# Optimization experiments

Measured on AMD Instinct MI355X. Metric: run time of the kernel, lower is better.

Reference implementation:

```python
import jax, jax.numpy as jnp
import numpy as np

B, N, D, YD = 256, 1024, 64, 2
EPS = 1e-7  # keras SCC epsilon clip


def interleave(x):
    # (B, L, ...): out[:,0::2]=first half, out[:,1::2]=second half
    b, L = x.shape[0], x.shape[1]
    a, c = x[:, : L // 2], x[:, L // 2:]
    return jnp.stack([a, c], axis=2).reshape((b, L) + x.shape[2:])


def block_interleave(x, scope):
    # tf.split into N//scope chunks of size `scope`, Interleave each, concat
    b, L = x.shape[0], x.shape[1]
    rest = x.shape[2:]
    xr = x.reshape((b, L // scope, 2, scope // 2) + rest)
    xr = jnp.swapaxes(xr, 2, 3)
    return xr.reshape((b, L) + rest)


def split_even_odd(x):
    # returns (odd, even) = (x[:,0::2], x[:,1::2])
    return x[:, 0::2], x[:, 1::2]


def mlp2(x, W1, b1, W2, b2):
    return jnp.dot(jax.nn.relu(jnp.dot(x, W1) + b1), W2) + b2


def emb2llr(e, W, b):
    return jax.nn.softmax(jnp.dot(e, W) + b, axis=-1)


def scce(v, p):
    # v: (B,L,1) int labels, p: (B,L,2) probs -> (B,L) per-element NLL
    pt = jnp.take_along_axis(p, v, axis=-1)[..., 0]
    return -jnp.log(jnp.clip(pt, EPS, 1.0))


def setup_inputs() -> dict:
    key = jax.random.key(0)
    ks = jax.random.split(key, 16)
    s = lambda fan: 1.0 / np.sqrt(fan)
    return {
        "x": jax.random.randint(ks[0], (B, N, 1), 0, 2, dtype=jnp.int32),
        "y": jax.random.normal(ks[1], (B, N, YD), dtype=jnp.float32),
        "emb_W": jax.random.normal(ks[2], (YD, D), dtype=jnp.float32) * s(YD),
        "emb_b": jnp.zeros((D,), jnp.float32),
        "lab_emb": jax.random.normal(ks[3], (2, D), dtype=jnp.float32) * s(D),
        "cn_W1": jax.random.normal(ks[4], (2 * D, D), dtype=jnp.float32) * s(2 * D),
        "cn_b1": jnp.zeros((D,), jnp.float32),
        "cn_W2": jax.random.normal(ks[5], (D, D), dtype=jnp.float32) * s(D),
        "cn_b2": jnp.zeros((D,), jnp.float32),
        "bn_W1": jax.random.normal(ks[6], (3 * D, D), dtype=jnp.float32) * s(3 * D),
        "bn_b1": jnp.zeros((D,), jnp.float32),
        "bn_W2": jax.random.normal(ks[7], (D, D), dtype=jnp.float32) * s(D),
        "bn_b2": jnp.zeros((D,), jnp.float32),
        "llr_W": jax.random.normal(ks[8], (D, 2), dtype=jnp.float32) * s(D),
        "llr_b": jnp.zeros((2,), jnp.float32),
    }


def reference(x, y, emb_W, emb_b, lab_emb, cn_W1, cn_b1, cn_W2, cn_b2,
              bn_W1, bn_b1, bn_W2, bn_b2, llr_W, llr_b):
    v = x.astype(jnp.int32)  # (B,N,1)
    e = jnp.dot(y, emb_W) + emb_b  # (B,N,D) observation embedding

    losses, preds, norms = [], [], []
    pred = emb2llr(e, llr_W, llr_b)
    losses.append(scce(v, pred))
    preds.append(pred)
    norms.append(jnp.linalg.norm(e, axis=-1))

    scope = 2
    while scope <= N:
        v_il = block_interleave(v, scope)
        v_odd, v_even = split_even_odd(v_il)
        v_xor = jnp.mod(v_odd + v_even, 2)  # (B,N/2,1)
        v_prime = interleave(jnp.concatenate((v_xor, v_even), axis=1))

        e_il = block_interleave(e, scope)
        e_odd, e_even = split_even_odd(e_il)  # (B,N/2,D) each
        v_xor_emb = lab_emb[v_xor[..., 0]]  # (B,N/2,D)

        e1_left = mlp2(jnp.concatenate((e_odd, e_even), axis=-1),
                       cn_W1, cn_b1, cn_W2, cn_b2)
        e1_right = mlp2(jnp.concatenate((e_odd, e_even, v_xor_emb), axis=-1),
                        bn_W1, bn_b1, bn_W2, bn_b2)
        e_prime = interleave(jnp.concatenate((e1_left, e1_right), axis=1))

        pred = emb2llr(e_prime, llr_W, llr_b)
        losses.append(scce(v_prime, pred))
        preds.append(pred)
        norms.append(jnp.linalg.norm(e_prime, axis=-1))

        v, e = v_prime, e_prime
        scope *= 2

    return (jnp.stack(losses, axis=-2),   # (B, S, N)
            jnp.stack(preds, axis=-2),    # (B, N, S, 2)
            jnp.stack(norms, axis=-2))    # (B, S, N)
```

## Files before the change

kernel.cpp:

```cpp
#include <hip/hip_runtime.h>
#include <hip/hip_bf16.h>

#define NB 256
#define NN 1024
#define NSTAGES 11
#define EPSF 1e-7f

typedef unsigned short u16;
typedef unsigned int u32;
typedef unsigned long long u64;
typedef __attribute__((ext_vector_type(8))) short short8;
typedef __attribute__((ext_vector_type(16))) float f32x16;

static constexpr size_t PRED_BASE = (size_t)NB * NSTAGES * NN;
static constexpr size_t NORM_BASE = PRED_BASE + (size_t)NB * NN * NSTAGES * 2;

static constexpr int LW_OFF = 24576;

#define WLDS_FR 30

static constexpr size_t STAGE_OFF = 131072;
static constexpr size_t PRED_F2_PER_B = (size_t)NSTAGES * NN;
static constexpr size_t PRED_BYTES = (size_t)NB * NSTAGES * NN * 2 * sizeof(float);
static constexpr size_t E9_OFF = STAGE_OFF + PRED_BYTES;
static constexpr size_t E9_BYTES = (size_t)512 * 65536;
static constexpr size_t VM_OFF = E9_OFF + E9_BYTES;
static constexpr size_t NEED_SPLIT = VM_OFF + (size_t)512 * 16 * sizeof(u32);
static constexpr size_t NEED_STAGED = STAGE_OFF + PRED_BYTES;

__device__ __forceinline__ u16 f2bf(float f) {
  unsigned u = __float_as_uint(f);
  unsigned r = (u + 0x7fffu + ((u >> 16) & 1u)) >> 16;
  return (u16)r;
}
__device__ __forceinline__ unsigned pack_bf2(float a, float b) {
  __hip_bfloat162 h = __float22bfloat162_rn(make_float2(a, b));
  return *(unsigned*)&h;
}
__device__ __forceinline__ u32 spread16(u32 v) {
  v = (v | (v << 8)) & 0x00FF00FFu;
  v = (v | (v << 4)) & 0x0F0F0F0Fu;
  v = (v | (v << 2)) & 0x33333333u;
  v = (v | (v << 1)) & 0x55555555u;
  return v;
}
template <bool STAGED>
__device__ __forceinline__ void emit_out(float* __restrict__ out, float* __restrict__ pred_ws,
                                         int b, int n, int s,
                                         float z0, float z1, float nrm2, int label) {
  float m  = fmaxf(z0, z1);
  float p0 = expf(z0 - m), p1 = expf(z1 - m);
  float inv = 1.0f / (p0 + p1);
  p0 *= inv; p1 *= inv;
  float pt = label ? p1 : p0;
  pt = fminf(fmaxf(pt, EPSF), 1.0f);
  out[((size_t)b * NSTAGES + s) * NN + n] = -logf(pt);
  if (STAGED) {
    ((float2*)pred_ws)[((size_t)b * NSTAGES + s) * NN + n] = make_float2(p0, p1);
  } else {
    size_t pb = PRED_BASE + (((size_t)b * NN + n) * NSTAGES + s) * 2;
    out[pb + 0] = p0;
    out[pb + 1] = p1;
  }
  out[NORM_BASE + ((size_t)b * NSTAGES + s) * NN + n] = sqrtf(nrm2);
}

__device__ __forceinline__ int eaddr(int row, int c16) {
  return row * 64 + (((c16) ^ (row & 7)) << 3);
}
__device__ __forceinline__ int eaddr32(int row, int m31) {
  return row * 64 + (((((m31) >> 2) ^ (row & 7)) << 3) | (((m31) & 3) << 1));
}

__global__ __launch_bounds__(256) void prep_kernel(
    const float* __restrict__ cn_W1, const float* __restrict__ bn_W1,
    const float* __restrict__ cn_W2, const float* __restrict__ bn_W2,
    const float* __restrict__ lab_emb, const float* __restrict__ llr_W,
    const float* __restrict__ bn_b1,
    u16* __restrict__ wfrag, float* __restrict__ labW_g) {
  int t = blockIdx.x * 256 + threadIdx.x;
  if (t < 3072) {
    int f = t >> 6, l = t & 63, h = l >> 5, c = l & 31;
    const float* src; int ks, nt;
    if (f < 16)      { src = cn_W1; ks = f >> 1; nt = f & 1; }
    else if (f < 32) { int g = f - 16; src = bn_W1; ks = g >> 1; nt = g & 1; }
    else if (f < 40) { int g = f - 32; src = cn_W2; ks = g >> 1; nt = g & 1; }
    else             { int g = f - 40; src = bn_W2; ks = g >> 1; nt = g & 1; }
    int col = 2 * c + nt;
    u16 vals[8];
    #pragma unroll
    for (int j = 0; j < 8; ++j) {
      int k = ks * 16 + h * 8 + j;
      vals[j] = f2bf(src[k * 64 + col]);
    }
    uint4 u;
    u.x = (unsigned)vals[0] | ((unsigned)vals[1] << 16);
    u.y = (unsigned)vals[2] | ((unsigned)vals[3] << 16);
    u.z = (unsigned)vals[4] | ((unsigned)vals[5] << 16);
    u.w = (unsigned)vals[6] | ((unsigned)vals[7] << 16);
    *(uint4*)(wfrag + (size_t)t * 8) = u;
  } else if (t < 3136) {
    int k = t - 3072;
    unsigned wv = (unsigned)f2bf(llr_W[k * 2]) | ((unsigned)f2bf(llr_W[k * 2 + 1]) << 16);
    ((unsigned*)(wfrag + LW_OFF))[k] = wv;
  } else if (t < 3264) {
    int idx = t - 3136;
    int v = idx >> 6, c = idx & 63;
    float acc = bn_b1[c];
    for (int d = 0; d < 64; ++d)
      acc = fmaf(lab_emb[v * 64 + d], bn_W1[(128 + d) * 64 + c], acc);
    labW_g[idx] = acc;
  }
}

__global__ __launch_bounds__(512) void pred_transpose_kernel(
    const float* __restrict__ pred_ws, float* __restrict__ out) {
  __shared__ float2 tb[NSTAGES * 1026];
  const int tid = threadIdx.x;
  const int b = blockIdx.x;
  const float2* src = (const float2*)pred_ws + (size_t)b * PRED_F2_PER_B;
  for (int i = tid; i < NSTAGES * NN; i += 512) {
    int s = i >> 10, n = i & (NN - 1);
    tb[s * 1026 + n] = src[i];
  }
  __syncthreads();
  float2* dst = (float2*)(out + PRED_BASE) + (size_t)b * PRED_F2_PER_B;
  for (int j = tid; j < NSTAGES * NN; j += 512) {
    int n = j / NSTAGES, s = j - n * NSTAGES;
    dst[j] = tb[s * 1026 + n];
  }
}

#define AFR(FI) (*(const short8*)(wlds + (FI) * 512 + ln * 8))
#define BFR(FI) (((FI) < WLDS_FR) ? *(const short8*)(wlds + (FI) * 512 + ln * 8) \
                                  : *(const short8*)(wfrag + (size_t)(FI) * 512 + ln * 8))

__global__ __launch_bounds__(512, 2) void polar_a_kernel(
    const int* __restrict__ x, const float* __restrict__ y,
    const float* __restrict__ emb_W, const float* __restrict__ emb_b,
    const u16* __restrict__ wfrag, const float* __restrict__ labW_g,
    const float* __restrict__ cn_b1, const float* __restrict__ cn_b2,
    const float* __restrict__ bn_b2, const float* __restrict__ llr_W,
    const float* __restrict__ llr_b, float* __restrict__ pred_ws,
    u16* __restrict__ e9_ws, u32* __restrict__ vm_ws,
    float* __restrict__ out) {
  __shared__ __align__(16) u16 eLh[512 * 64];
  __shared__ __align__(16) u16 wlds[48 * 512];
  __shared__ u32 lwL[64];
  __shared__ u32 vmask[2][16];
  __shared__ float labW[2][64];

  const int tid = threadIdx.x;
  const int w = tid >> 6, ln = tid & 63;
  const int m31 = ln & 31, h8 = ln >> 5;
  const int b = blockIdx.x >> 1, h = blockIdx.x & 1;

  for (int i = tid; i < 48 * 64; i += 512)
    ((uint4*)wlds)[i] = ((const uint4*)wfrag)[i];
  if (tid < 64) lwL[tid] = ((const u32*)(wfrag + LW_OFF))[tid];
  if (tid < 128) ((float*)labW)[tid] = labW_g[tid];

  const float lb0 = llr_b[0], lb1 = llr_b[1];
  const float2 cb1 = *(const float2*)(cn_b1 + 2 * m31);
  const float2 cb2 = *(const float2*)(cn_b2 + 2 * m31);
  const float2 bb2 = *(const float2*)(bn_b2 + 2 * m31);

  {
    int nl = tid;
    int n = 512 * h + nl;
    float2 yv = *(const float2*)(y + ((size_t)b * NN + n) * 2);
    float z0 = lb0, z1 = lb1, nr = 0.f;
    #pragma unroll
    for (int o8 = 0; o8 < 8; ++o8) {
      u32 vals[4];
      #pragma unroll
      for (int jj = 0; jj < 4; ++jj) {
        int o = o8 * 8 + jj * 2;
        float e0 = fmaf(yv.x, emb_W[o],     fmaf(yv.y, emb_W[64 + o],     emb_b[o]));
        float e1 = fmaf(yv.x, emb_W[o + 1], fmaf(yv.y, emb_W[64 + o + 1], emb_b[o + 1]));
        vals[jj] = pack_bf2(e0, e1);
        z0 = fmaf(e0, llr_W[o * 2 + 0], z0); z1 = fmaf(e0, llr_W[o * 2 + 1], z1);
        nr = fmaf(e0, e0, nr);
        z0 = fmaf(e1, llr_W[o * 2 + 2], z0); z1 = fmaf(e1, llr_W[o * 2 + 3], z1);
        nr = fmaf(e1, e1, nr);
      }
      uint4 q; q.x = vals[0]; q.y = vals[1]; q.z = vals[2]; q.w = vals[3];
      *(uint4*)(eLh + eaddr(nl, o8)) = q;
    }
    int v = x[(size_t)b * NN + n] & 1;
    emit_out<true>(out, pred_ws, b, n, 0, z0, z1, nr, v);
    u64 bm = __ballot(v != 0);
    if (ln == 0)  vmask[0][2 * w]     = (u32)bm;
    if (ln == 32) vmask[0][2 * w + 1] = (u32)(bm >> 32);
  }
  __syncthreads();

  const float2 lwv0 = *(const float2*)(&labW[0][2 * m31]);
  const float2 lwv1 = *(const float2*)(&labW[1][2 * m31]);

  #pragma unroll 1
  for (int s = 1; s <= 9; ++s) {
    const int sh = s - 1;
    const int half = 1 << sh;
    const u32* vmR = vmask[(s - 1) & 1];
    u32* vmW = vmask[s & 1];

    short8 Ao[4], Ae[4];
    int iog, ieg, iol, iel, vo, ve, vx;
    u32 bxs;
    {
      int i = 256 * h + 32 * w + m31;
      int g = i >> sh, u = i & (half - 1);
      iog = g * (half << 1) + u;
      ieg = iog + half;
      iol = iog & 511; iel = ieg & 511;
      #pragma unroll
      for (int f = 0; f < 4; ++f) {
        Ao[f] = *(const short8*)(eLh + eaddr(iol, f * 2 + h8));
        Ae[f] = *(const short8*)(eLh + eaddr(iel, f * 2 + h8));
      }
      vo = (vmR[iol >> 5] >> (iol & 31)) & 1;
      ve = (vmR[iel >> 5] >> (iel & 31)) & 1;
      vx = vo ^ ve;
      u32 bx = (u32)__ballot(vx != 0);
      u32 be = (u32)__ballot(ve != 0);
      bxs = bx;
      u32 lo = spread16(bx & 0xffffu) | (spread16(be & 0xffffu) << 1);
      u32 hi = spread16(bx >> 16) | (spread16(be >> 16) << 1);
      if (ln == 0) { vmW[2 * w] = lo; vmW[2 * w + 1] = hi; }
    }
    __syncthreads();

    if (s >= 2) {
      const uint4* lwq = (const uint4*)lwL;
      uint4 lq[4][2];
      #pragma unroll
      for (int f = 0; f < 4; ++f) {
        lq[f][0] = lwq[f * 4 + h8 * 2];
        lq[f][1] = lwq[f * 4 + h8 * 2 + 1];
      }
      #pragma unroll
      for (int side = 0; side < 2; ++side) {
        float z0 = 0.f, z1 = 0.f, nr = 0.f;
        #pragma unroll
        for (int f = 0; f < 4; ++f) {
          short8 av8 = side ? Ae[f] : Ao[f];
          #pragma unroll
          for (int j = 0; j < 8; ++j) {
            u32 pv = ((const u32*)&av8)[j >> 1];
            float val = __uint_as_float((j & 1) ? (pv & 0xffff0000u) : (pv << 16));
            u32 lwp = (j < 4) ? ((const u32*)&lq[f][0])[j] : ((const u32*)&lq[f][1])[j - 4];
            z0 = fmaf(val, __uint_as_float(lwp << 16), z0);
            z1 = fmaf(val, __uint_as_float(lwp & 0xffff0000u), z1);
            nr = fmaf(val, val, nr);
          }
        }
        z0 += __shfl_xor(z0, 32);
        z1 += __shfl_xor(z1, 32);
        nr += __shfl_xor(nr, 32);
        if (h8 == 0)
          emit_out<true>(out, pred_ws, b, side ? ieg : iog, s - 1,
                         z0 + lb0, z1 + lb1, nr, side ? ve : vo);
      }
    }

    f32x16 a0, a1;
    #pragma unroll
    for (int r = 0; r < 16; ++r) { a0[r] = cb1.x; a1[r] = cb1.y; }
    #pragma unroll
    for (int ks = 0; ks < 8; ++ks) {
      short8 B0 = AFR(ks * 2 + 0);
      short8 B1 = AFR(ks * 2 + 1);
      short8 a = (ks < 4) ? Ao[ks] : Ae[ks - 4];
      a0 = __builtin_amdgcn_mfma_f32_32x32x16_bf16(a, B0, a0, 0, 0, 0);
      a1 = __builtin_amdgcn_mfma_f32_32x32x16_bf16(a, B1, a1, 0, 0, 0);
    }
    {
      int obase = 64 * w;
      #pragma unroll
      for (int r = 0; r < 16; ++r) {
        int row = (r & 3) + 8 * (r >> 2) + 4 * h8;
        int R = obase + 2 * row;
        *(u32*)(eLh + eaddr32(R, m31)) =
            pack_bf2(fmaxf(a0[r], 0.f), fmaxf(a1[r], 0.f));
      }
    }

    #pragma unroll
    for (int r = 0; r < 16; ++r) {
      int row = (r & 3) + 8 * (r >> 2) + 4 * h8;
      int bit = (bxs >> row) & 1;
      a0[r] = bit ? lwv1.x : lwv0.x;
      a1[r] = bit ? lwv1.y : lwv0.y;
    }
    #pragma unroll
    for (int ks = 0; ks < 8; ++ks) {
      short8 B0 = AFR(16 + ks * 2 + 0);
      short8 B1 = AFR(16 + ks * 2 + 1);
      short8 a = (ks < 4) ? Ao[ks] : Ae[ks - 4];
      a0 = __builtin_amdgcn_mfma_f32_32x32x16_bf16(a, B0, a0, 0, 0, 0);
      a1 = __builtin_amdgcn_mfma_f32_32x32x16_bf16(a, B1, a1, 0, 0, 0);
    }
    {
      int obase = 64 * w;
      #pragma unroll
      for (int r = 0; r < 16; ++r) {
        int row = (r & 3) + 8 * (r >> 2) + 4 * h8;
        int R = obase + 2 * row + 1;
        *(u32*)(eLh + eaddr32(R, m31)) =
            pack_bf2(fmaxf(a0[r], 0.f), fmaxf(a1[r], 0.f));
      }
    }

    {
      short8 Hc[4];
      {
        int R = 64 * w + 2 * m31;
        #pragma unroll
        for (int f = 0; f < 4; ++f)
          Hc[f] = *(const short8*)(eLh + eaddr(R, f * 2 + h8));
      }
      f32x16 d0, d1;
      #pragma unroll
      for (int r = 0; r < 16; ++r) { d0[r] = cb2.x; d1[r] = cb2.y; }
      #pragma unroll
      for (int ks = 0; ks < 4; ++ks) {
        short8 B0 = AFR(32 + ks * 2 + 0);
        short8 B1 = AFR(32 + ks * 2 + 1);
        d0 = __builtin_amdgcn_mfma_f32_32x32x16_bf16(Hc[ks], B0, d0, 0, 0, 0);
        d1 = __builtin_amdgcn_mfma_f32_32x32x16_bf16(Hc[ks], B1, d1, 0, 0, 0);
      }
      int obase = 64 * w;
      #pragma unroll
      for (int r = 0; r < 16; ++r) {
        int row = (r & 3) + 8 * (r >> 2) + 4 * h8;
        int R = obase + 2 * row;
        *(u32*)(eLh + eaddr32(R, m31)) = pack_bf2(d0[r], d1[r]);
      }
    }

    {
      short8 Hb[4];
      {
        int R = 64 * w + 2 * m31 + 1;
        #pragma unroll
        for (int f = 0; f < 4; ++f)
          Hb[f] = *(const short8*)(eLh + eaddr(R, f * 2 + h8));
      }
      f32x16 d0, d1;
      #pragma unroll
      for (int r = 0; r < 16; ++r) { d0[r] = bb2.x; d1[r] = bb2.y; }
      #pragma unroll
      for (int ks = 0; ks < 4; ++ks) {
        short8 B0 = AFR(40 + ks * 2 + 0);
        short8 B1 = AFR(40 + ks * 2 + 1);
        d0 = __builtin_amdgcn_mfma_f32_32x32x16_bf16(Hb[ks], B0, d0, 0, 0, 0);
        d1 = __builtin_amdgcn_mfma_f32_32x32x16_bf16(Hb[ks], B1, d1, 0, 0, 0);
      }
      int obase = 64 * w;
      #pragma unroll
      for (int r = 0; r < 16; ++r) {
        int row = (r & 3) + 8 * (r >> 2) + 4 * h8;
        int R = obase + 2 * row + 1;
        *(u32*)(eLh + eaddr32(R, m31)) = pack_bf2(d0[r], d1[r]);
      }
    }
    __syncthreads();
  }

  {
    const uint4* src = (const uint4*)eLh;
    uint4* dst = (uint4*)(e9_ws + (size_t)(b * 2 + h) * 32768);
    for (int i = tid; i < 4096; i += 512) dst[i] = src[i];
    if (tid < 16) vm_ws[(b * 2 + h) * 16 + tid] = vmask[1][tid];
  }
}

__global__ __launch_bounds__(512, 2) void polar_b_kernel(
    const u16* __restrict__ wfrag, const float* __restrict__ labW_g,
    const float* __restrict__ cn_b1, const float* __restrict__ cn_b2,
    const float* __restrict__ bn_b2, const float* __restrict__ llr_b,
    float* __restrict__ pred_ws, const u16* __restrict__ e9_ws,
    const u32* __restrict__ vm_ws, float* __restrict__ out) {
  __shared__ __align__(16) u16 eL[NN * 64];
  __shared__ __align__(16) u16 wlds[WLDS_FR * 512];
  __shared__ u32 lwL[64];
  __shared__ u32 vmA[32];
  __shared__ u32 vmB[32];
  __shared__ float labW[2][64];

  const int tid = threadIdx.x;
  const int w = tid >> 6, ln = tid & 63;
  const int m31 = ln & 31, h8 = ln >> 5;
  const int b = blockIdx.x;

  for (int i = tid; i < WLDS_FR * 64; i += 512)
    ((uint4*)wlds)[i] = ((const uint4*)wfrag)[i];
  if (tid < 64) lwL[tid] = ((const u32*)(wfrag + LW_OFF))[tid];
  if (tid < 128) ((float*)labW)[tid] = labW_g[tid];
  if (tid < 32) vmA[tid] = vm_ws[b * 32 + tid];

  const float lb0 = llr_b[0], lb1 = llr_b[1];
  const float2 cb1 = *(const float2*)(cn_b1 + 2 * m31);
  const float2 cb2 = *(const float2*)(cn_b2 + 2 * m31);
  const float2 bb2 = *(const float2*)(bn_b2 + 2 * m31);
  __syncthreads();

  const float2 lwv0 = *(const float2*)(&labW[0][2 * m31]);
  const float2 lwv1 = *(const float2*)(&labW[1][2 * m31]);

  const u16* e9a = e9_ws + (size_t)(b * 2 + 0) * 32768;
  const u16* e9b = e9_ws + (size_t)(b * 2 + 1) * 32768;

  short8 Ao[2][4], Ae[2][4];
  int io[2], ie[2], vo[2], ve[2], vx[2];
  u32 bxs[2];
  #pragma unroll
  for (int t = 0; t < 2; ++t) {
    int i = 64 * w + 32 * t + m31;
    io[t] = i; ie[t] = i + 512;
    #pragma unroll
    for (int f = 0; f < 4; ++f) {
      Ao[t][f] = *(const short8*)(e9a + eaddr(i, f * 2 + h8));
      Ae[t][f] = *(const short8*)(e9b + eaddr(i, f * 2 + h8));
    }
    vo[t] = (vmA[i >> 5] >> (i & 31)) & 1;
    ve[t] = (vmA[(i >> 5) + 16] >> (i & 31)) & 1;
    vx[t] = vo[t] ^ ve[t];
    u32 bx = (u32)__ballot(vx[t] != 0);
    u32 be = (u32)__ballot(ve[t] != 0);
    bxs[t] = bx;
    u32 lo = spread16(bx & 0xffffu) | (spread16(be & 0xffffu) << 1);
    u32 hi = spread16(bx >> 16) | (spread16(be >> 16) << 1);
    if (ln == 0) { vmB[4 * w + 2 * t] = lo; vmB[4 * w + 2 * t + 1] = hi; }
  }
  __syncthreads();

  {
    const uint4* lwq = (const uint4*)lwL;
    uint4 lq[4][2];
    #pragma unroll
    for (int f = 0; f < 4; ++f) {
      lq[f][0] = lwq[f * 4 + h8 * 2];
      lq[f][1] = lwq[f * 4 + h8 * 2 + 1];
    }
    #pragma unroll
    for (int t = 0; t < 2; ++t) {
      #pragma unroll
      for (int side = 0; side < 2; ++side) {
        float z0 = 0.f, z1 = 0.f, nr = 0.f;
        #pragma unroll
        for (int f = 0; f < 4; ++f) {
          short8 av8 = side ? Ae[t][f] : Ao[t][f];
          #pragma unroll
          for (int j = 0; j < 8; ++j) {
            u32 pv = ((const u32*)&av8)[j >> 1];
            float val = __uint_as_float((j & 1) ? (pv & 0xffff0000u) : (pv << 16));
            u32 lwp = (j < 4) ? ((const u32*)&lq[f][0])[j] : ((const u32*)&lq[f][1])[j - 4];
            z0 = fmaf(val, __uint_as_float(lwp << 16), z0);
            z1 = fmaf(val, __uint_as_float(lwp & 0xffff0000u), z1);
            nr = fmaf(val, val, nr);
          }
        }
        z0 += __shfl_xor(z0, 32);
        z1 += __shfl_xor(z1, 32);
        nr += __shfl_xor(nr, 32);
        if (h8 == 0)
          emit_out<true>(out, pred_ws, b, side ? ie[t] : io[t], 9,
                         z0 + lb0, z1 + lb1, nr, side ? ve[t] : vo[t]);
      }
    }
  }

  f32x16 a0[2], a1[2];
  #pragma unroll
  for (int t = 0; t < 2; ++t)
    #pragma unroll
    for (int r = 0; r < 16; ++r) { a0[t][r] = cb1.x; a1[t][r] = cb1.y; }
  #pragma unroll
  for (int ks = 0; ks < 8; ++ks) {
    short8 B0 = BFR(ks * 2 + 0);
    short8 B1 = BFR(ks * 2 + 1);
    #pragma unroll
    for (int t = 0; t < 2; ++t) {
      short8 a = (ks < 4) ? Ao[t][ks] : Ae[t][ks - 4];
      a0[t] = __builtin_amdgcn_mfma_f32_32x32x16_bf16(a, B0, a0[t], 0, 0, 0);
      a1[t] = __builtin_amdgcn_mfma_f32_32x32x16_bf16(a, B1, a1[t], 0, 0, 0);
    }
  }
  #pragma unroll
  for (int t = 0; t < 2; ++t) {
    int obase = 128 * w + 64 * t;
    #pragma unroll
    for (int r = 0; r < 16; ++r) {
      int row = (r & 3) + 8 * (r >> 2) + 4 * h8;
      int R = obase + 2 * row;
      *(u32*)(eL + eaddr32(R, m31)) =
          pack_bf2(fmaxf(a0[t][r], 0.f), fmaxf(a1[t][r], 0.f));
    }
  }

  #pragma unroll
  for (int t = 0; t < 2; ++t)
    #pragma unroll
    for (int r = 0; r < 16; ++r) {
      int row = (r & 3) + 8 * (r >> 2) + 4 * h8;
      int bit = (bxs[t] >> row) & 1;
      a0[t][r] = bit ? lwv1.x : lwv0.x;
      a1[t][r] = bit ? lwv1.y : lwv0.y;
    }
  #pragma unroll
  for (int ks = 0; ks < 8; ++ks) {
    short8 B0 = BFR(16 + ks * 2 + 0);
    short8 B1 = BFR(16 + ks * 2 + 1);
    #pragma unroll
    for (int t = 0; t < 2; ++t) {
      short8 a = (ks < 4) ? Ao[t][ks] : Ae[t][ks - 4];
      a0[t] = __builtin_amdgcn_mfma_f32_32x32x16_bf16(a, B0, a0[t], 0, 0, 0);
      a1[t] = __builtin_amdgcn_mfma_f32_32x32x16_bf16(a, B1, a1[t], 0, 0, 0);
    }
  }
  #pragma unroll
  for (int t = 0; t < 2; ++t) {
    int obase = 128 * w + 64 * t;
    #pragma unroll
    for (int r = 0; r < 16; ++r) {
      int row = (r & 3) + 8 * (r >> 2) + 4 * h8;
      int R = obase + 2 * row + 1;
      *(u32*)(eL + eaddr32(R, m31)) =
          pack_bf2(fmaxf(a0[t][r], 0.f), fmaxf(a1[t][r], 0.f));
    }
  }

  {
    short8 Hc[2][4];
    #pragma unroll
    for (int t = 0; t < 2; ++t) {
      int R = 128 * w + 64 * t + 2 * m31;
      #pragma unroll
      for (int f = 0; f < 4; ++f)
        Hc[t][f] = *(const short8*)(eL + eaddr(R, f * 2 + h8));
    }
    f32x16 d0[2], d1[2];
    #pragma unroll
    for (int t = 0; t < 2; ++t)
      #pragma unroll
      for (int r = 0; r < 16; ++r) { d0[t][r] = cb2.x; d1[t][r] = cb2.y; }
    #pragma unroll
    for (int ks = 0; ks < 4; ++ks) {
      short8 B0 = BFR(32 + ks * 2 + 0);
      short8 B1 = BFR(32 + ks * 2 + 1);
      #pragma unroll
      for (int t = 0; t < 2; ++t) {
        d0[t] = __builtin_amdgcn_mfma_f32_32x32x16_bf16(Hc[t][ks], B0, d0[t], 0, 0, 0);
        d1[t] = __builtin_amdgcn_mfma_f32_32x32x16_bf16(Hc[t][ks], B1, d1[t], 0, 0, 0);
      }
    }
    #pragma unroll
    for (int t = 0; t < 2; ++t) {
      int obase = 128 * w + 64 * t;
      #pragma unroll
      for (int r = 0; r < 16; ++r) {
        int row = (r & 3) + 8 * (r >> 2) + 4 * h8;
        int R = obase + 2 * row;
        *(u32*)(eL + eaddr32(R, m31)) = pack_bf2(d0[t][r], d1[t][r]);
      }
    }
  }

  {
    short8 Hb[2][4];
    #pragma unroll
    for (int t = 0; t < 2; ++t) {
      int R = 128 * w + 64 * t + 2 * m31 + 1;
      #pragma unroll
      for (int f = 0; f < 4; ++f)
        Hb[t][f] = *(const short8*)(eL + eaddr(R, f * 2 + h8));
    }
    f32x16 d0[2], d1[2];
    #pragma unroll
    for (int t = 0; t < 2; ++t)
      #pragma unroll
      for (int r = 0; r < 16; ++r) { d0[t][r] = bb2.x; d1[t][r] = bb2.y; }
    #pragma unroll
    for (int ks = 0; ks < 4; ++ks) {
      short8 B0 = BFR(40 + ks * 2 + 0);
      short8 B1 = BFR(40 + ks * 2 + 1);
      #pragma unroll
      for (int t = 0; t < 2; ++t) {
        d0[t] = __builtin_amdgcn_mfma_f32_32x32x16_bf16(Hb[t][ks], B0, d0[t], 0, 0, 0);
        d1[t] = __builtin_amdgcn_mfma_f32_32x32x16_bf16(Hb[t][ks], B1, d1[t], 0, 0, 0);
      }
    }
    #pragma unroll
    for (int t = 0; t < 2; ++t) {
      int obase = 128 * w + 64 * t;
      #pragma unroll
      for (int r = 0; r < 16; ++r) {
        int row = (r & 3) + 8 * (r >> 2) + 4 * h8;
        int R = obase + 2 * row + 1;
        *(u32*)(eL + eaddr32(R, m31)) = pack_bf2(d0[t][r], d1[t][r]);
      }
    }
  }
  __syncthreads();

  {
    const uint4* lwq = (const uint4*)lwL;
    uint4 lq[4][2];
    #pragma unroll
    for (int f = 0; f < 4; ++f) {
      lq[f][0] = lwq[f * 4 + h8 * 2];
      lq[f][1] = lwq[f * 4 + h8 * 2 + 1];
    }
    #pragma unroll
    for (int it = 0; it < 4; ++it) {
      int n = 128 * w + 32 * it + m31;
      float z0 = 0.f, z1 = 0.f, nr = 0.f;
      #pragma unroll
      for (int f = 0; f < 4; ++f) {
        short8 av8 = *(const short8*)(eL + eaddr(n, f * 2 + h8));
        #pragma unroll
        for (int j = 0; j < 8; ++j) {
          u32 pv = ((const u32*)&av8)[j >> 1];
          float val = __uint_as_float((j & 1) ? (pv & 0xffff0000u) : (pv << 16));
          u32 lwp = (j < 4) ? ((const u32*)&lq[f][0])[j] : ((const u32*)&lq[f][1])[j - 4];
          z0 = fmaf(val, __uint_as_float(lwp << 16), z0);
          z1 = fmaf(val, __uint_as_float(lwp & 0xffff0000u), z1);
          nr = fmaf(val, val, nr);
        }
      }
      z0 += __shfl_xor(z0, 32);
      z1 += __shfl_xor(z1, 32);
      nr += __shfl_xor(nr, 32);
      int lab = (vmB[n >> 5] >> (n & 31)) & 1;
      if (h8 == 0)
        emit_out<true>(out, pred_ws, b, n, NSTAGES - 1, z0 + lb0, z1 + lb1, nr, lab);
    }
  }
}

template <int STAGED>
__global__ __launch_bounds__(512, 2) void polar_mono_kernel(
    const int* __restrict__ x, const float* __restrict__ y,
    const float* __restrict__ emb_W, const float* __restrict__ emb_b,
    const u16* __restrict__ wfrag, const float* __restrict__ labW_g,
    const float* __restrict__ cn_b1, const float* __restrict__ cn_b2,
    const float* __restrict__ bn_b2, const float* __restrict__ llr_W,
    const float* __restrict__ llr_b, float* __restrict__ pred_ws,
    float* __restrict__ out) {
  __shared__ __align__(16) u16 eL[NN * 64];
  __shared__ __align__(16) u16 wlds[WLDS_FR * 512];
  __shared__ u32 lwL[64];
  __shared__ u32 vmask[2][32];
  __shared__ float labW[2][64];

  const int tid = threadIdx.x;
  const int w = tid >> 6, ln = tid & 63;
  const int m31 = ln & 31, h8 = ln >> 5;
  const int b = blockIdx.x;

  for (int i = tid; i < WLDS_FR * 64; i += 512)
    ((uint4*)wlds)[i] = ((const uint4*)wfrag)[i];
  if (tid < 64) lwL[tid] = ((const u32*)(wfrag + LW_OFF))[tid];
  if (tid < 128) ((float*)labW)[tid] = labW_g[tid];

  const float lb0 = llr_b[0], lb1 = llr_b[1];
  const float2 cb1 = *(const float2*)(cn_b1 + 2 * m31);
  const float2 cb2 = *(const float2*)(cn_b2 + 2 * m31);
  const float2 bb2 = *(const float2*)(bn_b2 + 2 * m31);

  #pragma unroll
  for (int rep = 0; rep < 2; ++rep) {
    int n = rep * 512 + tid;
    float2 yv = *(const float2*)(y + ((size_t)b * NN + n) * 2);
    float z0 = lb0, z1 = lb1, nr = 0.f;
    #pragma unroll
    for (int o8 = 0; o8 < 8; ++o8) {
      u32 vals[4];
      #pragma unroll
      for (int jj = 0; jj < 4; ++jj) {
        int o = o8 * 8 + jj * 2;
        float e0 = fmaf(yv.x, emb_W[o],     fmaf(yv.y, emb_W[64 + o],     emb_b[o]));
        float e1 = fmaf(yv.x, emb_W[o + 1], fmaf(yv.y, emb_W[64 + o + 1], emb_b[o + 1]));
        vals[jj] = pack_bf2(e0, e1);
        z0 = fmaf(e0, llr_W[o * 2 + 0], z0); z1 = fmaf(e0, llr_W[o * 2 + 1], z1);
        nr = fmaf(e0, e0, nr);
        z0 = fmaf(e1, llr_W[o * 2 + 2], z0); z1 = fmaf(e1, llr_W[o * 2 + 3], z1);
        nr = fmaf(e1, e1, nr);
      }
      uint4 q; q.x = vals[0]; q.y = vals[1]; q.z = vals[2]; q.w = vals[3];
      *(uint4*)(eL + eaddr(n, o8)) = q;
    }
    int v = x[(size_t)b * NN + n] & 1;
    emit_out<STAGED != 0>(out, pred_ws, b, n, 0, z0, z1, nr, v);
    u64 bm = __ballot(v != 0);
    if (ln == 0)  vmask[0][rep * 16 + 2 * w]     = (u32)bm;
    if (ln == 32) vmask[0][rep * 16 + 2 * w + 1] = (u32)(bm >> 32);
  }
  __syncthreads();

  const float2 lwv0 = *(const float2*)(&labW[0][2 * m31]);
  const float2 lwv1 = *(const float2*)(&labW[1][2 * m31]);

  #pragma unroll 1
  for (int s = 1; s <= 10; ++s) {
    const int sh = s - 1;
    const int half = 1 << sh;
    const u32* vmR = vmask[(s - 1) & 1];
    u32* vmW = vmask[s & 1];

    short8 Ao[2][4], Ae[2][4];
    int io[2], ie[2], vo[2], ve[2], vx[2];
    u32 bxs[2];
    #pragma unroll
    for (int t = 0; t < 2; ++t) {
      int i = 64 * w + 32 * t + m31;
      int g = i >> sh, u = i & (half - 1);
      io[t] = g * (half << 1) + u;
      ie[t] = io[t] + half;
      #pragma unroll
      for (int f = 0; f < 4; ++f) {
        Ao[t][f] = *(const short8*)(eL + eaddr(io[t], f * 2 + h8));
        Ae[t][f] = *(const short8*)(eL + eaddr(ie[t], f * 2 + h8));
      }
      vo[t] = (vmR[io[t] >> 5] >> (io[t] & 31)) & 1;
      ve[t] = (vmR[ie[t] >> 5] >> (ie[t] & 31)) & 1;
      vx[t] = vo[t] ^ ve[t];
      u32 bx = (u32)__ballot(vx[t] != 0);
      u32 be = (u32)__ballot(ve[t] != 0);
      bxs[t] = bx;
      u32 lo = spread16(bx & 0xffffu) | (spread16(be & 0xffffu) << 1);
      u32 hi = spread16(bx >> 16) | (spread16(be >> 16) << 1);
      if (ln == 0) { vmW[4 * w + 2 * t] = lo; vmW[4 * w + 2 * t + 1] = hi; }
    }
    __syncthreads();

    if (s >= 2) {
      const uint4* lwq = (const uint4*)lwL;
      uint4 lq[4][2];
      #pragma unroll
      for (int f = 0; f < 4; ++f) {
        lq[f][0] = lwq[f * 4 + h8 * 2];
        lq[f][1] = lwq[f * 4 + h8 * 2 + 1];
      }
      #pragma unroll
      for (int t = 0; t < 2; ++t) {
        #pragma unroll
        for (int side = 0; side < 2; ++side) {
          float z0 = 0.f, z1 = 0.f, nr = 0.f;
          #pragma unroll
          for (int f = 0; f < 4; ++f) {
            short8 av8 = side ? Ae[t][f] : Ao[t][f];
            #pragma unroll
            for (int j = 0; j < 8; ++j) {
              u32 pv = ((const u32*)&av8)[j >> 1];
              float val = __uint_as_float((j & 1) ? (pv & 0xffff0000u) : (pv << 16));
              u32 lwp = (j < 4) ? ((const u32*)&lq[f][0])[j] : ((const u32*)&lq[f][1])[j - 4];
              z0 = fmaf(val, __uint_as_float(lwp << 16), z0);
              z1 = fmaf(val, __uint_as_float(lwp & 0xffff0000u), z1);
              nr = fmaf(val, val, nr);
            }
          }
          z0 += __shfl_xor(z0, 32);
          z1 += __shfl_xor(z1, 32);
          nr += __shfl_xor(nr, 32);
          if (h8 == 0)
            emit_out<STAGED != 0>(out, pred_ws, b, side ? ie[t] : io[t], s - 1,
                                  z0 + lb0, z1 + lb1, nr, side ? ve[t] : vo[t]);
        }
      }
    }

    f32x16 a0[2], a1[2];
    #pragma unroll
    for (int t = 0; t < 2; ++t)
      #pragma unroll
      for (int r = 0; r < 16; ++r) { a0[t][r] = cb1.x; a1[t][r] = cb1.y; }
    #pragma unroll
    for (int ks = 0; ks < 8; ++ks) {
      short8 B0 = BFR(ks * 2 + 0);
      short8 B1 = BFR(ks * 2 + 1);
      #pragma unroll
      for (int t = 0; t < 2; ++t) {
        short8 a = (ks < 4) ? Ao[t][ks] : Ae[t][ks - 4];
        a0[t] = __builtin_amdgcn_mfma_f32_32x32x16_bf16(a, B0, a0[t], 0, 0, 0);
        a1[t] = __builtin_amdgcn_mfma_f32_32x32x16_bf16(a, B1, a1[t], 0, 0, 0);
      }
    }
    #pragma unroll
    for (int t = 0; t < 2; ++t) {
      int obase = 128 * w + 64 * t;
      #pragma unroll
      for (int r = 0; r < 16; ++r) {
        int row = (r & 3) + 8 * (r >> 2) + 4 * h8;
        int R = obase + 2 * row;
        *(u32*)(eL + eaddr32(R, m31)) =
            pack_bf2(fmaxf(a0[t][r], 0.f), fmaxf(a1[t][r], 0.f));
      }
    }

    #pragma unroll
    for (int t = 0; t < 2; ++t)
      #pragma unroll
      for (int r = 0; r < 16; ++r) {
        int row = (r & 3) + 8 * (r >> 2) + 4 * h8;
        int bit = (bxs[t] >> row) & 1;
        a0[t][r] = bit ? lwv1.x : lwv0.x;
        a1[t][r] = bit ? lwv1.y : lwv0.y;
      }
    #pragma unroll
    for (int ks = 0; ks < 8; ++ks) {
      short8 B0 = BFR(16 + ks * 2 + 0);
      short8 B1 = BFR(16 + ks * 2 + 1);
      #pragma unroll
      for (int t = 0; t < 2; ++t) {
        short8 a = (ks < 4) ? Ao[t][ks] : Ae[t][ks - 4];
        a0[t] = __builtin_amdgcn_mfma_f32_32x32x16_bf16(a, B0, a0[t], 0, 0, 0);
        a1[t] = __builtin_amdgcn_mfma_f32_32x32x16_bf16(a, B1, a1[t], 0, 0, 0);
      }
    }
    #pragma unroll
    for (int t = 0; t < 2; ++t) {
      int obase = 128 * w + 64 * t;
      #pragma unroll
      for (int r = 0; r < 16; ++r) {
        int row = (r & 3) + 8 * (r >> 2) + 4 * h8;
        int R = obase + 2 * row + 1;
        *(u32*)(eL + eaddr32(R, m31)) =
            pack_bf2(fmaxf(a0[t][r], 0.f), fmaxf(a1[t][r], 0.f));
      }
    }

    {
      short8 Hc[2][4];
      #pragma unroll
      for (int t = 0; t < 2; ++t) {
        int R = 128 * w + 64 * t + 2 * m31;
        #pragma unroll
        for (int f = 0; f < 4; ++f)
          Hc[t][f] = *(const short8*)(eL + eaddr(R, f * 2 + h8));
      }
      f32x16 d0[2], d1[2];
      #pragma unroll
      for (int t = 0; t < 2; ++t)
        #pragma unroll
        for (int r = 0; r < 16; ++r) { d0[t][r] = cb2.x; d1[t][r] = cb2.y; }
      #pragma unroll
      for (int ks = 0; ks < 4; ++ks) {
        short8 B0 = BFR(32 + ks * 2 + 0);
        short8 B1 = BFR(32 + ks * 2 + 1);
        #pragma unroll
        for (int t = 0; t < 2; ++t) {
          d0[t] = __builtin_amdgcn_mfma_f32_32x32x16_bf16(Hc[t][ks], B0, d0[t], 0, 0, 0);
          d1[t] = __builtin_amdgcn_mfma_f32_32x32x16_bf16(Hc[t][ks], B1, d1[t], 0, 0, 0);
        }
      }
      #pragma unroll
      for (int t = 0; t < 2; ++t) {
        int obase = 128 * w + 64 * t;
        #pragma unroll
        for (int r = 0; r < 16; ++r) {
          int row = (r & 3) + 8 * (r >> 2) + 4 * h8;
          int R = obase + 2 * row;
          *(u32*)(eL + eaddr32(R, m31)) = pack_bf2(d0[t][r], d1[t][r]);
        }
      }
    }

    {
      short8 Hb[2][4];
      #pragma unroll
      for (int t = 0; t < 2; ++t) {
        int R = 128 * w + 64 * t + 2 * m31 + 1;
        #pragma unroll
        for (int f = 0; f < 4; ++f)
          Hb[t][f] = *(const short8*)(eL + eaddr(R, f * 2 + h8));
      }
      f32x16 d0[2], d1[2];
      #pragma unroll
      for (int t = 0; t < 2; ++t)
        #pragma unroll
        for (int r = 0; r < 16; ++r) { d0[t][r] = bb2.x; d1[t][r] = bb2.y; }
      #pragma unroll
      for (int ks = 0; ks < 4; ++ks) {
        short8 B0 = BFR(40 + ks * 2 + 0);
        short8 B1 = BFR(40 + ks * 2 + 1);
        #pragma unroll
        for (int t = 0; t < 2; ++t) {
          d0[t] = __builtin_amdgcn_mfma_f32_32x32x16_bf16(Hb[t][ks], B0, d0[t], 0, 0, 0);
          d1[t] = __builtin_amdgcn_mfma_f32_32x32x16_bf16(Hb[t][ks], B1, d1[t], 0, 0, 0);
        }
      }
      #pragma unroll
      for (int t = 0; t < 2; ++t) {
        int obase = 128 * w + 64 * t;
        #pragma unroll
        for (int r = 0; r < 16; ++r) {
          int row = (r & 3) + 8 * (r >> 2) + 4 * h8;
          int R = obase + 2 * row + 1;
          *(u32*)(eL + eaddr32(R, m31)) = pack_bf2(d0[t][r], d1[t][r]);
        }
      }
    }
    __syncthreads();
  }

  {
    const uint4* lwq = (const uint4*)lwL;
    uint4 lq[4][2];
    #pragma unroll
    for (int f = 0; f < 4; ++f) {
      lq[f][0] = lwq[f * 4 + h8 * 2];
      lq[f][1] = lwq[f * 4 + h8 * 2 + 1];
    }
    #pragma unroll
    for (int it = 0; it < 4; ++it) {
      int n = 128 * w + 32 * it + m31;
      float z0 = 0.f, z1 = 0.f, nr = 0.f;
      #pragma unroll
      for (int f = 0; f < 4; ++f) {
        short8 av8 = *(const short8*)(eL + eaddr(n, f * 2 + h8));
        #pragma unroll
        for (int j = 0; j < 8; ++j) {
          u32 pv = ((const u32*)&av8)[j >> 1];
          float val = __uint_as_float((j & 1) ? (pv & 0xffff0000u) : (pv << 16));
          u32 lwp = (j < 4) ? ((const u32*)&lq[f][0])[j] : ((const u32*)&lq[f][1])[j - 4];
          z0 = fmaf(val, __uint_as_float(lwp << 16), z0);
          z1 = fmaf(val, __uint_as_float(lwp & 0xffff0000u), z1);
          nr = fmaf(val, val, nr);
        }
      }
      z0 += __shfl_xor(z0, 32);
      z1 += __shfl_xor(z1, 32);
      nr += __shfl_xor(nr, 32);
      int lab = (vmask[0][n >> 5] >> (n & 31)) & 1;
      if (h8 == 0)
        emit_out<STAGED != 0>(out, pred_ws, b, n, NSTAGES - 1, z0 + lb0, z1 + lb1, nr, lab);
    }
  }
}

extern "C" void kernel_launch(void* const* d_in, const int* in_sizes, int n_in,
                              void* d_out, int out_size, void* d_ws, size_t ws_size,
                              hipStream_t stream) {
  const int*   x      = (const int*)d_in[0];
  const float* y      = (const float*)d_in[1];
  const float* emb_W  = (const float*)d_in[2];
  const float* emb_b  = (const float*)d_in[3];
  const float* labemb = (const float*)d_in[4];
  const float* cn_W1  = (const float*)d_in[5];
  const float* cn_b1  = (const float*)d_in[6];
  const float* cn_W2  = (const float*)d_in[7];
  const float* cn_b2  = (const float*)d_in[8];
  const float* bn_W1  = (const float*)d_in[9];
  const float* bn_b1  = (const float*)d_in[10];
  const float* bn_W2  = (const float*)d_in[11];
  const float* bn_b2  = (const float*)d_in[12];
  const float* llr_W  = (const float*)d_in[13];
  const float* llr_b  = (const float*)d_in[14];
  float* out = (float*)d_out;

  u16* wfrag = (u16*)d_ws;
  float* labW_g = (float*)((char*)d_ws + 65536);
  float* pred_ws = (float*)((char*)d_ws + STAGE_OFF);
  u16* e9_ws = (u16*)((char*)d_ws + E9_OFF);
  u32* vm_ws = (u32*)((char*)d_ws + VM_OFF);

  prep_kernel<<<13, 256, 0, stream>>>(cn_W1, bn_W1, cn_W2, bn_W2, labemb, llr_W,
                                      bn_b1, wfrag, labW_g);
  if (ws_size >= NEED_SPLIT) {
    polar_a_kernel<<<2 * NB, 512, 0, stream>>>(x, y, emb_W, emb_b, wfrag, labW_g,
                                               cn_b1, cn_b2, bn_b2, llr_W, llr_b,
                                               pred_ws, e9_ws, vm_ws, out);
    polar_b_kernel<<<NB, 512, 0, stream>>>(wfrag, labW_g, cn_b1, cn_b2, bn_b2,
                                           llr_b, pred_ws, e9_ws, vm_ws, out);
    pred_transpose_kernel<<<NB, 512, 0, stream>>>(pred_ws, out);
  } else if (ws_size >= NEED_STAGED) {
    polar_mono_kernel<1><<<NB, 512, 0, stream>>>(x, y, emb_W, emb_b, wfrag, labW_g,
                                                 cn_b1, cn_b2, bn_b2, llr_W, llr_b,
                                                 pred_ws, out);
    pred_transpose_kernel<<<NB, 512, 0, stream>>>(pred_ws, out);
  } else {
    polar_mono_kernel<0><<<NB, 512, 0, stream>>>(x, y, emb_W, emb_b, wfrag, labW_g,
                                                 cn_b1, cn_b2, bn_b2, llr_W, llr_b,
                                                 pred_ws, out);
  }
}
```

Before: 252.8 us.

## Pad polar_a LDS rows and fuse pred transpose into polar_b tail

Pads the per-row stride of the polar_a shared embedding buffer from 64 to 72 elements while keeping the XOR swizzle, aiming to cut LDS bank conflicts on the MFMA operand loads and scatter stores. The e9 export loop is adapted to de-pad rows. The separate pred_transpose kernel launch is removed and its work is done at the end of polar_b, reusing the eL LDS buffer as the transpose tile. This saves one launch and one global round trip of scheduling, but raises polar_a LDS usage, which could lower occupancy, and adds a serialized tail to polar_b.

```diff
diff --git a/kernel.cpp b/kernel.cpp
--- a/kernel.cpp
+++ b/kernel.cpp
@@ -71,6 +71,12 @@
 __device__ __forceinline__ int eaddr32(int row, int m31) {
   return row * 64 + (((((m31) >> 2) ^ (row & 7)) << 3) | (((m31) & 3) << 1));
 }
+__device__ __forceinline__ int eaddrA(int row, int c16) {
+  return row * 72 + (((c16) ^ (row & 7)) << 3);
+}
+__device__ __forceinline__ int eaddr32A(int row, int m31) {
+  return row * 72 + (((((m31) >> 2) ^ (row & 7)) << 3) | (((m31) & 3) << 1));
+}
 
 __global__ __launch_bounds__(256) void prep_kernel(
     const float* __restrict__ cn_W1, const float* __restrict__ bn_W1,
@@ -144,7 +150,7 @@
     const float* __restrict__ llr_b, float* __restrict__ pred_ws,
     u16* __restrict__ e9_ws, u32* __restrict__ vm_ws,
     float* __restrict__ out) {
-  __shared__ __align__(16) u16 eLh[512 * 64];
+  __shared__ __align__(16) u16 eLh[512 * 72];
   __shared__ __align__(16) u16 wlds[48 * 512];
   __shared__ u32 lwL[64];
   __shared__ u32 vmask[2][16];
@@ -185,7 +191,7 @@
         nr = fmaf(e1, e1, nr);
       }
       uint4 q; q.x = vals[0]; q.y = vals[1]; q.z = vals[2]; q.w = vals[3];
-      *(uint4*)(eLh + eaddr(nl, o8)) = q;
+      *(uint4*)(eLh + eaddrA(nl, o8)) = q;
     }
     int v = x[(size_t)b * NN + n] & 1;
     emit_out<true>(out, pred_ws, b, n, 0, z0, z1, nr, v);
@@ -216,8 +222,8 @@
       iol = iog & 511; iel = ieg & 511;
       #pragma unroll
       for (int f = 0; f < 4; ++f) {
-        Ao[f] = *(const short8*)(eLh + eaddr(iol, f * 2 + h8));
-        Ae[f] = *(const short8*)(eLh + eaddr(iel, f * 2 + h8));
+        Ao[f] = *(const short8*)(eLh + eaddrA(iol, f * 2 + h8));
+        Ae[f] = *(const short8*)(eLh + eaddrA(iel, f * 2 + h8));
       }
       vo = (vmR[iol >> 5] >> (iol & 31)) & 1;
       ve = (vmR[iel >> 5] >> (iel & 31)) & 1;
@@ -281,7 +287,7 @@
       for (int r = 0; r < 16; ++r) {
         int row = (r & 3) + 8 * (r >> 2) + 4 * h8;
         int R = obase + 2 * row;
-        *(u32*)(eLh + eaddr32(R, m31)) =
+        *(u32*)(eLh + eaddr32A(R, m31)) =
             pack_bf2(fmaxf(a0[r], 0.f), fmaxf(a1[r], 0.f));
       }
     }
@@ -307,7 +313,7 @@
       for (int r = 0; r < 16; ++r) {
         int row = (r & 3) + 8 * (r >> 2) + 4 * h8;
         int R = obase + 2 * row + 1;
-        *(u32*)(eLh + eaddr32(R, m31)) =
+        *(u32*)(eLh + eaddr32A(R, m31)) =
             pack_bf2(fmaxf(a0[r], 0.f), fmaxf(a1[r], 0.f));
       }
     }
@@ -318,7 +324,7 @@
         int R = 64 * w + 2 * m31;
         #pragma unroll
         for (int f = 0; f < 4; ++f)
-          Hc[f] = *(const short8*)(eLh + eaddr(R, f * 2 + h8));
+          Hc[f] = *(const short8*)(eLh + eaddrA(R, f * 2 + h8));
       }
       f32x16 d0, d1;
       #pragma unroll
@@ -335,7 +341,7 @@
       for (int r = 0; r < 16; ++r) {
         int row = (r & 3) + 8 * (r >> 2) + 4 * h8;
         int R = obase + 2 * row;
-        *(u32*)(eLh + eaddr32(R, m31)) = pack_bf2(d0[r], d1[r]);
+        *(u32*)(eLh + eaddr32A(R, m31)) = pack_bf2(d0[r], d1[r]);
       }
     }
 
@@ -345,7 +351,7 @@
         int R = 64 * w + 2 * m31 + 1;
         #pragma unroll
         for (int f = 0; f < 4; ++f)
-          Hb[f] = *(const short8*)(eLh + eaddr(R, f * 2 + h8));
+          Hb[f] = *(const short8*)(eLh + eaddrA(R, f * 2 + h8));
       }
       f32x16 d0, d1;
       #pragma unroll
@@ -362,16 +368,18 @@
       for (int r = 0; r < 16; ++r) {
         int row = (r & 3) + 8 * (r >> 2) + 4 * h8;
         int R = obase + 2 * row + 1;
-        *(u32*)(eLh + eaddr32(R, m31)) = pack_bf2(d0[r], d1[r]);
+        *(u32*)(eLh + eaddr32A(R, m31)) = pack_bf2(d0[r], d1[r]);
       }
     }
     __syncthreads();
   }
 
   {
-    const uint4* src = (const uint4*)eLh;
-    uint4* dst = (uint4*)(e9_ws + (size_t)(b * 2 + h) * 32768);
-    for (int i = tid; i < 4096; i += 512) dst[i] = src[i];
+    u16* dst = e9_ws + (size_t)(b * 2 + h) * 32768;
+    for (int idx = tid; idx < 4096; idx += 512) {
+      int r = idx >> 3, c = idx & 7;
+      *(uint4*)(dst + r * 64 + c * 8) = *(const uint4*)(eLh + r * 72 + c * 8);
+    }
     if (tid < 16) vm_ws[(b * 2 + h) * 16 + tid] = vmask[1][tid];
   }
 }
@@ -636,6 +644,22 @@
       int lab = (vmB[n >> 5] >> (n & 31)) & 1;
       if (h8 == 0)
         emit_out<true>(out, pred_ws, b, n, NSTAGES - 1, z0 + lb0, z1 + lb1, nr, lab);
+    }
+  }
+
+  __syncthreads();
+  {
+    float2* tb = (float2*)eL;
+    const float2* srcp = (const float2*)pred_ws + (size_t)b * PRED_F2_PER_B;
+    for (int i = tid; i < NSTAGES * NN; i += 512) {
+      int s = i >> 10, n = i & (NN - 1);
+      tb[s * 1026 + n] = srcp[i];
+    }
+    __syncthreads();
+    float2* dstp = (float2*)(out + PRED_BASE) + (size_t)b * PRED_F2_PER_B;
+    for (int j = tid; j < NSTAGES * NN; j += 512) {
+      int n = j / NSTAGES, s = j - n * NSTAGES;
+      dstp[j] = tb[s * 1026 + n];
     }
   }
 }
@@ -975,7 +999,6 @@
                                                pred_ws, e9_ws, vm_ws, out);
     polar_b_kernel<<<NB, 512, 0, stream>>>(wfrag, labW_g, cn_b1, cn_b2, bn_b2,
                                            llr_b, pred_ws, e9_ws, vm_ws, out);
-    pred_transpose_kernel<<<NB, 512, 0, stream>>>(pred_ws, out);
   } else if (ws_size >= NEED_STAGED) {
     polar_mono_kernel<1><<<NB, 512, 0, stream>>>(x, y, emb_W, emb_b, wfrag, labW_g,
                                                  cn_b1, cn_b2, bn_b2, llr_W, llr_b,
```

Result: no change. 257.2 us (+1.7%).
